# Kernel tuning notes

Measured on AMD Instinct MI355X. Metric: run time of the kernel, lower is better.

## Reference

```python
import jax, jax.numpy as jnp
import numpy as np

NUM, NUM_TOP, COBJ = 32, 32, 4   # num = MBS*ncobj, num_top, cobj_size = k//2
B, D, H = 300, 256, 256          # bag_size, feature dim, relation hidden
K_OBJ = 8                        # k (output cobj size)
FEA0 = 2 * NUM * COBJ            # orig_fea leading dim = MBS*K with K=2*ncobj*cobj_size


def setup_inputs() -> dict:
    key = jax.random.key(0)
    ks = jax.random.split(key, 8)
    return {
        "orig_fea": jax.random.normal(ks[0], (FEA0, B, D), dtype=jnp.float32),
        "ind0": jax.random.randint(ks[1], (NUM, NUM_TOP, COBJ), 0, B, dtype=jnp.int32),
        "ind1": jax.random.randint(ks[2], (NUM, NUM_TOP, COBJ), 0, B, dtype=jnp.int32),
        "k": K_OBJ,
        "W1a": jax.random.normal(ks[3], (D, H), dtype=jnp.float32) * (1.0 / np.sqrt(D)),
        "W1b": jax.random.normal(ks[4], (D, H), dtype=jnp.float32) * (1.0 / np.sqrt(D)),
        "b1": jnp.zeros((H,), dtype=jnp.float32),
        "W2": jax.random.normal(ks[5], (H, 1), dtype=jnp.float32) * (1.0 / np.sqrt(H)),
        "b2": jnp.zeros((1,), dtype=jnp.float32),
    }


def reference(orig_fea, ind0, ind1, k, W1a, W1b, b1, W2, b2):
    num, num_top, cobj = ind0.shape
    bag = orig_fea.shape[1]
    d = orig_fea.shape[2]
    # create_ids: stride bag_size over cobj positions -> [num, L], L = num_top*cobj
    off = (bag * jnp.arange(cobj, dtype=ind0.dtype))
    ids0 = (ind0 + off).reshape(num, -1)
    ids1 = (ind1 + off).reshape(num, -1)
    # rsolo_fea = reshape(orig_fea, [num, 2, pool, D]); pool = cobj*bag
    pool = (orig_fea.shape[0] * bag) // (2 * num)
    rsolo = orig_fea.reshape(num, 2, pool, d)
    # gather per-side features (dedup+inverse-gather in the original is an
    # optimization; direct gather yields the identical score matrix)
    f0 = jnp.take_along_axis(rsolo[:, 0], ids0[..., None], axis=1)  # [num, L, D]
    f1 = jnp.take_along_axis(rsolo[:, 1], ids1[..., None], axis=1)  # [num, L, D]
    # relation unit: score(a,b) = MLP(concat(f0_a, f1_b)) -> [num, L, L, 1]
    h0 = jnp.einsum('nad,dh->nah', f0, W1a)          # [num, L, H]
    h1 = jnp.einsum('nbd,dh->nbh', f1, W1b)          # [num, L, H]
    h = jax.nn.relu(h0[:, :, None, :] + h1[:, None, :, :] + b1)  # [num, L, L, H]
    scores = jnp.einsum('nabh,ho->nabo', h, W2) + b2              # [num, L, L, 1]
    # sum_kxk_patches with patch size k//2
    kp = k // 2
    L = num_top * cobj
    hk = L // kp
    scores = scores.reshape(num, hk, kp, hk, kp, 1).sum(axis=(2, 4))  # [num, m, l, 1]
    m = l = num_top
    scores = scores.reshape(num, m * l, 1)
    # get_pairs
    pairs = jnp.stack(jnp.meshgrid(jnp.arange(m, dtype=jnp.int32),
                                   jnp.arange(l, dtype=jnp.int32), indexing='ij'),
                      axis=-1).reshape(1, m * l, 2)
    pairs = jnp.broadcast_to(pairs, (num, m * l, 2))
    return scores, pairs
```

## Files before the change

kernel.cpp:

```cpp
#include <hip/hip_runtime.h>

#define NUMB 32
#define LL   128
#define POOL 1200
#define BAG  300
#define DD   256
#define HH   256
#define NS   (NUMB*32*32)

using bf16x8 = __bf16    __attribute__((ext_vector_type(8)));
using f32x4  = float     __attribute__((ext_vector_type(4)));
using fp16x2 = __fp16    __attribute__((ext_vector_type(2)));
using h16x2  = _Float16  __attribute__((ext_vector_type(2)));
using h16x8  = _Float16  __attribute__((ext_vector_type(8)));

typedef const __attribute__((address_space(1))) unsigned int* gas_t;
typedef       __attribute__((address_space(3))) unsigned int* las_t;

static __device__ __forceinline__ unsigned short f2bf(float x) {
    unsigned u = __float_as_uint(x);
    return (unsigned short)((u + 0x7FFFu + ((u >> 16) & 1u)) >> 16);
}

static __device__ __forceinline__ float pkh(float a, float b) {
    fp16x2 p = __builtin_amdgcn_cvt_pkrtz(a, b);
    return __builtin_bit_cast(float, p);
}

__global__ __launch_bounds__(256) void k_prep(
    const float* __restrict__ W1a, const float* __restrict__ W1b,
    const float* __restrict__ b2,
    unsigned short* __restrict__ WtP, float* __restrict__ out)
{
    const int blk = blockIdx.x, t = threadIdx.x;
    if (blk < 32) {
        const int side = blk >> 4, kc = blk & 15;
        const float* W = side ? W1b : W1a;
        __shared__ float T[16][257];
        const int row = t >> 4, c = t & 15;
#pragma unroll
        for (int i = 0; i < 4; ++i) {
            int col4 = c + i * 16;
            float4 v = *(const float4*)(W + (size_t)(kc * 16 + row) * HH + col4 * 4);
            T[row][col4 * 4 + 0] = v.x; T[row][col4 * 4 + 1] = v.y;
            T[row][col4 * 4 + 2] = v.z; T[row][col4 * 4 + 3] = v.w;
        }
        __syncthreads();
        const int n = t, ht = n >> 6, nn = n & 63;
#pragma unroll
        for (int j = 0; j < 2; ++j) {
            unsigned short tmp[8] __attribute__((aligned(16)));
#pragma unroll
            for (int e = 0; e < 8; ++e) tmp[e] = f2bf(T[j * 8 + e][n]);
            int U = kc * 2 + j;
            int pos = U ^ (nn & 7);
            size_t unit = ((size_t)((side * 4 + ht) * 64 + nn)) * 32 + pos;
            *(float4*)(WtP + unit * 8) = *(float4*)tmp;
        }
    } else {
        int i = (blk - 32) * 256 + t;
        if (i < NS) {
            out[i] = 16.0f * b2[0];
        } else if (i < 3 * NS) {
            int j = i - NS;
            int p = (j >> 1) & 1023;
            out[i] = (j & 1) ? (float)(p & 31) : (float)(p >> 5);
        }
    }
}

__global__ __launch_bounds__(256) void k_gemm(
    const float* __restrict__ fea,
    const int*   __restrict__ ind0,
    const int*   __restrict__ ind1,
    const float* __restrict__ b1,
    const unsigned short* __restrict__ WtP,
    unsigned short* __restrict__ Hh)
{
    __shared__ unsigned short As[64 * 256] __attribute__((aligned(16)));
    __shared__ unsigned short Bs[64 * 256] __attribute__((aligned(16)));

    int b = blockIdx.x;
    const int ht = b & 3, rt = b >> 2;
    const int side = rt >> 6;
    const int R0 = rt * 64;
    const int t = threadIdx.x, w = t >> 6, lane = t & 63;

    const unsigned short* Wbase = WtP + ((size_t)(side * 4 + ht)) * 64 * 256;
#pragma unroll
    for (int i = 0; i < 8; ++i) {
        int chunk = w * 8 + i;
        __builtin_amdgcn_global_load_lds(
            (gas_t)(const void*)(Wbase + chunk * 512 + lane * 8),
            (las_t)(void*)(As + chunk * 512),
            16, 0, 0);
    }

    {
        const int lr = t >> 2;
        const int g = R0 + lr;
        const int rs = g & 4095, n_ = rs >> 7, a_ = rs & 127;
        const int id = (side ? ind1 : ind0)[n_ * LL + a_] + BAG * (a_ & 3);
        const float* arow = fea + (size_t)((n_ * 2 + side) * POOL + id) * DD;
        const int sw = lr & 7;
#pragma unroll
        for (int j0 = 0; j0 < 16; ++j0) {
            int jj = j0 * 4 + (t & 3);
            float4 v = *(const float4*)(arow + jj * 4);
            unsigned short tmp[4] __attribute__((aligned(8)));
            tmp[0] = f2bf(v.x); tmp[1] = f2bf(v.y);
            tmp[2] = f2bf(v.z); tmp[3] = f2bf(v.w);
            int u = jj >> 1, pos = u ^ sw;
            *(double*)&Bs[lr * 256 + pos * 8 + (jj & 1) * 4] = *(double*)tmp;
        }
    }
    __syncthreads();

    const int l15 = lane & 15, q = lane >> 4;
    f32x4 acc[4] = {};
#pragma unroll
    for (int kk = 0; kk < 8; ++kk) {
        const int u = kk * 4 + q;
        const int hr = w * 16 + l15;
        bf16x8 af = *(const bf16x8*)&As[hr * 256 + (u ^ (hr & 7)) * 8];
        bf16x8 bf[4];
#pragma unroll
        for (int rb = 0; rb < 4; ++rb) {
            int r = rb * 16 + l15;
            bf[rb] = *(const bf16x8*)&Bs[r * 256 + (u ^ (r & 7)) * 8];
        }
#pragma unroll
        for (int rb = 0; rb < 4; ++rb)
            acc[rb] = __builtin_amdgcn_mfma_f32_16x16x32_bf16(af, bf[rb], acc[rb], 0, 0, 0);
    }

    const int hbase = ht * 64 + w * 16 + q * 4;
    float4 bias = make_float4(0.f, 0.f, 0.f, 0.f);
    if (side == 0) bias = *(const float4*)(b1 + hbase);
#pragma unroll
    for (int rb = 0; rb < 4; ++rb) {
        int frow = R0 + rb * 16 + l15;
        float2 pk;
        pk.x = pkh(acc[rb][0] + bias.x, acc[rb][1] + bias.y);
        pk.y = pkh(acc[rb][2] + bias.z, acc[rb][3] + bias.w);
        *(float2*)&Hh[(size_t)frow * HH + hbase] = pk;
    }
}

__global__ __launch_bounds__(256) void k_pair(
    const unsigned short* __restrict__ Hh,
    const float* __restrict__ W2,
    float*       __restrict__ out)
{
    __shared__ unsigned short s0[64 * 64] __attribute__((aligned(16)));
    __shared__ unsigned short s1[64 * 64] __attribute__((aligned(16)));
    __shared__ unsigned short w2s[64]     __attribute__((aligned(16)));

    int b = blockIdx.x;
    const int hs = b & 3;  b >>= 2;
    const int jt = b & 1;  b >>= 1;
    const int it = b & 1;  b >>= 1;
    const int n  = b;
    const int t = threadIdx.x, w = t >> 6, lane = t & 63;

    const size_t base0 = ((size_t)(n * LL) + it * 64) * HH + hs * 64;
    const size_t base1 = ((size_t)(NUMB * LL + n * LL) + jt * 64) * HH + hs * 64;

    {
        const int lrow = lane >> 3, posslot = lane & 7;
#pragma unroll
        for (int i = 0; i < 2; ++i) {
            int chunk = w * 2 + i;
            int row = chunk * 8 + lrow;
            int f = posslot ^ ((row >> 2) & 7);
            __builtin_amdgcn_global_load_lds(
                (gas_t)(const void*)(Hh + base0 + (size_t)row * HH + f * 8),
                (las_t)(void*)(s0 + chunk * 512), 16, 0, 0);
            __builtin_amdgcn_global_load_lds(
                (gas_t)(const void*)(Hh + base1 + (size_t)row * HH + f * 8),
                (las_t)(void*)(s1 + chunk * 512), 16, 0, 0);
        }
    }
    if (t < 16) {
        float4 v = *(const float4*)(W2 + hs * 64 + t * 4);
        float2 pk;
        pk.x = pkh(v.x, v.y);
        pk.y = pkh(v.z, v.w);
        *(float2*)&w2s[t * 4] = pk;
    }
    __syncthreads();

    const int jl = t & 15, il = t >> 4;
    float acc[4][4] = {{0.f,0.f,0.f,0.f},{0.f,0.f,0.f,0.f},
                       {0.f,0.f,0.f,0.f},{0.f,0.f,0.f,0.f}};

#pragma unroll
    for (int f = 0; f < 8; ++f) {
        h16x8 wv = *(const h16x8*)&w2s[f * 8];
        const h16x2* wp = (const h16x2*)&wv;
        h16x8 av[4], bv[4];
#pragma unroll
        for (int r = 0; r < 4; ++r)
            av[r] = *(const h16x8*)&s0[(il * 4 + r) * 64 + (f ^ (il & 7)) * 8];
#pragma unroll
        for (int s = 0; s < 4; ++s)
            bv[s] = *(const h16x8*)&s1[(jl * 4 + s) * 64 + (f ^ (jl & 7)) * 8];
        const h16x8 zero = {0, 0, 0, 0, 0, 0, 0, 0};
#pragma unroll
        for (int r = 0; r < 4; ++r)
#pragma unroll
            for (int s = 0; s < 4; ++s) {
                h16x8 sum = av[r] + bv[s];
                sum = __builtin_elementwise_max(sum, zero);
                const h16x2* sp = (const h16x2*)&sum;
#pragma unroll
                for (int u = 0; u < 4; ++u)
                    acc[r][s] = __builtin_amdgcn_fdot2(sp[u], wp[u], acc[r][s], false);
            }
    }

    float total = 0.f;
#pragma unroll
    for (int r = 0; r < 4; ++r)
#pragma unroll
        for (int s = 0; s < 4; ++s) total += acc[r][s];

    atomicAdd(out + n * 1024 + (it * 16 + il) * 32 + jt * 16 + jl, total);
}

extern "C" void kernel_launch(void* const* d_in, const int* in_sizes, int n_in,
                              void* d_out, int out_size, void* d_ws, size_t ws_size,
                              hipStream_t stream)
{
    const float* fea  = (const float*)d_in[0];
    const int*   ind0 = (const int*)  d_in[1];
    const int*   ind1 = (const int*)  d_in[2];
    const float* W1a  = (const float*)d_in[4];
    const float* W1b  = (const float*)d_in[5];
    const float* b1   = (const float*)d_in[6];
    const float* W2   = (const float*)d_in[7];
    const float* b2   = (const float*)d_in[8];
    float* out = (float*)d_out;

    unsigned short* WtP = (unsigned short*)d_ws;
    unsigned short* Hh  = (unsigned short*)((char*)d_ws + 512 * 1024);

    hipLaunchKernelGGL(k_prep, dim3(416), dim3(256), 0, stream,
                       W1a, W1b, b2, WtP, out);
    hipLaunchKernelGGL(k_gemm, dim3(512), dim3(256), 0, stream,
                       fea, ind0, ind1, b1, WtP, Hh);
    hipLaunchKernelGGL(k_pair, dim3(512), dim3(256), 0, stream,
                       Hh, W2, out);
}
```

Measured before the change: 131.2 us.

## Replace atomic H-split accumulation with in-block reduction in pair kernel

The pair kernel now gives each block a 32x32 row tile and the full hidden dimension, split across the four waves. Partial sums are reduced through shared memory and written with plain stores, which removes the global atomics and the need to pre-initialize the output with the bias. The prep kernel now only writes the pairs section using float4 stores, so its grid is much smaller. Each block loads full 256-wide rows (more LDS per block) and pays an extra barrier and reduction step.

```diff
diff --git a/kernel.cpp b/kernel.cpp
--- a/kernel.cpp
+++ b/kernel.cpp
@@ -29,7 +29,6 @@
 
 __global__ __launch_bounds__(256) void k_prep(
     const float* __restrict__ W1a, const float* __restrict__ W1b,
-    const float* __restrict__ b2,
     unsigned short* __restrict__ WtP, float* __restrict__ out)
 {
     const int blk = blockIdx.x, t = threadIdx.x;
@@ -58,14 +57,11 @@
             *(float4*)(WtP + unit * 8) = *(float4*)tmp;
         }
     } else {
-        int i = (blk - 32) * 256 + t;
-        if (i < NS) {
-            out[i] = 16.0f * b2[0];
-        } else if (i < 3 * NS) {
-            int j = i - NS;
-            int p = (j >> 1) & 1023;
-            out[i] = (j & 1) ? (float)(p & 31) : (float)(p >> 5);
-        }
+        int G = (blk - 32) * 256 + t;
+        int local = G & 511;
+        float i = (float)(local >> 4);
+        float c0 = (float)((2 * local) & 31);
+        ((float4*)(out + NS))[G] = make_float4(i, c0, i, c0 + 1.0f);
     }
 }
 
@@ -150,39 +146,40 @@
 __global__ __launch_bounds__(256) void k_pair(
     const unsigned short* __restrict__ Hh,
     const float* __restrict__ W2,
+    const float* __restrict__ b2,
     float*       __restrict__ out)
 {
-    __shared__ unsigned short s0[64 * 64] __attribute__((aligned(16)));
-    __shared__ unsigned short s1[64 * 64] __attribute__((aligned(16)));
-    __shared__ unsigned short w2s[64]     __attribute__((aligned(16)));
+    __shared__ unsigned short s0[32 * 256] __attribute__((aligned(16)));
+    __shared__ unsigned short s1[32 * 256] __attribute__((aligned(16)));
+    __shared__ unsigned short w2s[256]     __attribute__((aligned(16)));
+    __shared__ float sred[256];
 
     int b = blockIdx.x;
-    const int hs = b & 3;  b >>= 2;
-    const int jt = b & 1;  b >>= 1;
-    const int it = b & 1;  b >>= 1;
+    const int jt = b & 3;  b >>= 2;
+    const int it = b & 3;  b >>= 2;
     const int n  = b;
     const int t = threadIdx.x, w = t >> 6, lane = t & 63;
 
-    const size_t base0 = ((size_t)(n * LL) + it * 64) * HH + hs * 64;
-    const size_t base1 = ((size_t)(NUMB * LL + n * LL) + jt * 64) * HH + hs * 64;
+    const size_t base0 = ((size_t)(n * LL) + it * 32) * HH;
+    const size_t base1 = ((size_t)(NUMB * LL + n * LL) + jt * 32) * HH;
 
     {
-        const int lrow = lane >> 3, posslot = lane & 7;
-#pragma unroll
-        for (int i = 0; i < 2; ++i) {
-            int chunk = w * 2 + i;
-            int row = chunk * 8 + lrow;
-            int f = posslot ^ ((row >> 2) & 7);
+        const int pos = lane & 31, rhalf = lane >> 5;
+#pragma unroll
+        for (int i = 0; i < 4; ++i) {
+            int rowbase = w * 8 + i * 2;
+            int row = rowbase + rhalf;
+            int f = pos ^ ((row >> 2) & 7);
             __builtin_amdgcn_global_load_lds(
                 (gas_t)(const void*)(Hh + base0 + (size_t)row * HH + f * 8),
-                (las_t)(void*)(s0 + chunk * 512), 16, 0, 0);
+                (las_t)(void*)(s0 + rowbase * 256), 16, 0, 0);
             __builtin_amdgcn_global_load_lds(
                 (gas_t)(const void*)(Hh + base1 + (size_t)row * HH + f * 8),
-                (las_t)(void*)(s1 + chunk * 512), 16, 0, 0);
-        }
-    }
-    if (t < 16) {
-        float4 v = *(const float4*)(W2 + hs * 64 + t * 4);
+                (las_t)(void*)(s1 + rowbase * 256), 16, 0, 0);
+        }
+    }
+    if (t < 64) {
+        float4 v = *(const float4*)(W2 + t * 4);
         float2 pk;
         pk.x = pkh(v.x, v.y);
         pk.y = pkh(v.z, v.w);
@@ -190,21 +187,21 @@
     }
     __syncthreads();
 
-    const int jl = t & 15, il = t >> 4;
+    const int il = (t >> 3) & 7, jl = t & 7;
     float acc[4][4] = {{0.f,0.f,0.f,0.f},{0.f,0.f,0.f,0.f},
                        {0.f,0.f,0.f,0.f},{0.f,0.f,0.f,0.f}};
 
 #pragma unroll
     for (int f = 0; f < 8; ++f) {
-        h16x8 wv = *(const h16x8*)&w2s[f * 8];
+        h16x8 wv = *(const h16x8*)&w2s[(w * 8 + f) * 8];
         const h16x2* wp = (const h16x2*)&wv;
         h16x8 av[4], bv[4];
 #pragma unroll
         for (int r = 0; r < 4; ++r)
-            av[r] = *(const h16x8*)&s0[(il * 4 + r) * 64 + (f ^ (il & 7)) * 8];
+            av[r] = *(const h16x8*)&s0[(il * 4 + r) * 256 + (w * 8 + (f ^ il)) * 8];
 #pragma unroll
         for (int s = 0; s < 4; ++s)
-            bv[s] = *(const h16x8*)&s1[(jl * 4 + s) * 64 + (f ^ (jl & 7)) * 8];
+            bv[s] = *(const h16x8*)&s1[(jl * 4 + s) * 256 + (w * 8 + (f ^ jl)) * 8];
         const h16x8 zero = {0, 0, 0, 0, 0, 0, 0, 0};
 #pragma unroll
         for (int r = 0; r < 4; ++r)
@@ -225,7 +222,16 @@
 #pragma unroll
         for (int s = 0; s < 4; ++s) total += acc[r][s];
 
-    atomicAdd(out + n * 1024 + (it * 16 + il) * 32 + jt * 16 + jl, total);
+    sred[t] = total;
+    __syncthreads();
+
+    if (t < 64) {
+        float sum = sred[t] + sred[t + 64] + sred[t + 128] + sred[t + 192]
+                  + 16.0f * b2[0];
+        int i = it * 8 + (t >> 3);
+        int j = jt * 8 + (t & 7);
+        out[n * 1024 + i * 32 + j] = sum;
+    }
 }
 
 extern "C" void kernel_launch(void* const* d_in, const int* in_sizes, int n_in,
@@ -245,10 +251,10 @@
     unsigned short* WtP = (unsigned short*)d_ws;
     unsigned short* Hh  = (unsigned short*)((char*)d_ws + 512 * 1024);
 
-    hipLaunchKernelGGL(k_prep, dim3(416), dim3(256), 0, stream,
-                       W1a, W1b, b2, WtP, out);
+    hipLaunchKernelGGL(k_prep, dim3(96), dim3(256), 0, stream,
+                       W1a, W1b, WtP, out);
     hipLaunchKernelGGL(k_gemm, dim3(512), dim3(256), 0, stream,
                        fea, ind0, ind1, b1, WtP, Hh);
     hipLaunchKernelGGL(k_pair, dim3(512), dim3(256), 0, stream,
-                       Hh, W2, out);
-}
+                       Hh, W2, b2, out);
+}
```

Measured after the change: 130.9 us. No clear change (-0.3%).
